# Performance work log

Hardware: AMD Instinct MI355X
Metric: run time of the kernel (lower is better)

## Reference

```python
import jax, jax.numpy as jnp
import numpy as np

B, HQ, HKV, QL, SL = 2, 32, 8, 1024, 4096
HEAD_DIM, HALF, ROPE, RANK = 128, 64, 64, 512


def setup_inputs() -> dict:
    key = jax.random.key(0)
    ks = jax.random.split(key, 6)
    return {
        "Q": jax.random.normal(ks[0], (B, HQ, QL, HEAD_DIM), jnp.float32),
        "C_kv_t2": jax.random.normal(ks[1], (B, SL, RANK), jnp.float32),
        "K_rope_t2": jax.random.normal(ks[2], (B, HKV, SL, ROPE), jnp.float32),
        "U_l": jax.random.normal(ks[3], (HALF, HALF), jnp.float32) / 8.0,
        "W_UK": jax.random.normal(ks[4], (HEAD_DIM - ROPE, RANK), jnp.float32) / 8.0,
        "W_UV": jax.random.normal(ks[5], (RANK, HEAD_DIM), jnp.float32) / 8.0,
    }


def reference(Q, C_kv_t2, K_rope_t2, U_l, W_UK, W_UV):
    # --- absorb_and_score ---
    # Rotate each half of Q by U_l (applied as x @ U_l.T)
    Qx, Qy = Q[..., :HALF], Q[..., HALF:]
    Q_rot = jnp.concatenate([Qx @ U_l.T, Qy @ U_l.T], axis=-1)  # [B,HQ,QL,HEAD_DIM]
    Q_rope = Q_rot[..., :ROPE]                                   # [B,HQ,QL,ROPE]
    Q_nope = Q_rot[..., ROPE:]                                   # [B,HQ,QL,nope_dim]
    Q_abs = Q_nope @ W_UK                                        # [B,HQ,QL,RANK]
    scores_nope = jnp.einsum('bhqr,bsr->bhqs', Q_abs, C_kv_t2)   # [B,HQ,QL,SL]
    # GQA: group q-heads per kv-head instead of materializing repeat_interleave
    g = HQ // HKV
    Qr_g = Q_rope.reshape(B, HKV, g, QL, ROPE)
    scores_rope = jnp.einsum('bkgqr,bksr->bkgqs', Qr_g, K_rope_t2)
    scores = scores_nope + scores_rope.reshape(B, HQ, QL, SL)
    # --- softmax glue + decompress_value ---
    weights = jax.nn.softmax(scores, axis=-1)                    # [B,HQ,QL,SL]
    out_latent = jnp.einsum('bhqs,bsr->bhqr', weights, C_kv_t2)  # [B,HQ,QL,RANK]
    out = out_latent @ W_UV                                      # [B,HQ,QL,HEAD_DIM]
    return out
```

## Files before the change

kernel.cpp:

```cpp
#include <hip/hip_runtime.h>
#include <stdint.h>

#define B_N   2
#define HQ_N  32
#define HKV_N 8
#define QL_N  1024
#define SL_N  4096
#define DH_N  128
#define ROPE_N 64
#define RANK_N 512

typedef _Float16 f16;
typedef _Float16 half8 __attribute__((ext_vector_type(8)));
typedef float floatx16 __attribute__((ext_vector_type(16)));
typedef int int2v __attribute__((ext_vector_type(2)));

union H8 { half8 h; uint64_t q[2]; };
union H4 { f16 h[4]; uint64_t q; };
union PKU { f16 h[2]; uint32_t u; };
union BFU { uint32_t u[4]; half8 h; };

__global__ __launch_bounds__(256) void k_convert(const float* __restrict__ C,
                                                 const float* __restrict__ Kr,
                                                 f16* __restrict__ Cf,
                                                 f16* __restrict__ Krf) {
  const size_t NC = (size_t)B_N * SL_N * RANK_N;
  size_t idx = ((size_t)blockIdx.x * 256 + threadIdx.x) * 8;
  const float* src;
  f16* dst;
  if (idx < NC) { src = C + idx;        dst = Cf + idx; }
  else          { src = Kr + (idx - NC); dst = Krf + (idx - NC); }
  float4 a = *(const float4*)(src);
  float4 b = *(const float4*)(src + 4);
  H8 o;
  o.h[0] = (f16)a.x; o.h[1] = (f16)a.y; o.h[2] = (f16)a.z; o.h[3] = (f16)a.w;
  o.h[4] = (f16)b.x; o.h[5] = (f16)b.y; o.h[6] = (f16)b.z; o.h[7] = (f16)b.w;
  *(half8*)dst = o.h;
}

__global__ __launch_bounds__(256) void k_m2(const float* __restrict__ Ul,
                                            f16* __restrict__ M2T2) {
  int idx = blockIdx.x * 256 + threadIdx.x;
  int c = idx >> 7, d = idx & 127;
  float v = 0.f;
  if (c < 64) { if (d >= 64) v = Ul[c * 64 + (d - 64)]; }
  else        { if (d < 64)  v = Ul[(c - 64) * 64 + d]; }
  M2T2[idx] = (f16)v;
}

__global__ __launch_bounds__(256) void k_qeff(const float* __restrict__ Q,
                                              const f16* __restrict__ M2T2,
                                              f16* __restrict__ Qeff2) {
  __shared__ __align__(16) f16 qs[128 * 132];
  int t = threadIdx.x;
  int wave = t >> 6, lane = t & 63, l31 = lane & 31, lhi = lane >> 5;
  size_t m0 = (size_t)blockIdx.x * 128;
#pragma unroll
  for (int i = 0; i < 16; i++) {
    int flat = i * 256 + t; int row = flat >> 5, seg = flat & 31;
    float4 v = *(const float4*)(Q + (m0 + row) * DH_N + seg * 4);
    H4 o; o.h[0] = (f16)v.x; o.h[1] = (f16)v.y; o.h[2] = (f16)v.z; o.h[3] = (f16)v.w;
    *(uint64_t*)(qs + row * 132 + seg * 4) = o.q;
  }
  __syncthreads();
  floatx16 acc[4];
#pragma unroll
  for (int ct = 0; ct < 4; ct++)
#pragma unroll
    for (int r = 0; r < 16; r++) acc[ct][r] = 0.f;
#pragma unroll
  for (int kk = 0; kk < 8; ++kk) {
    H8 af;
    const uint64_t* pa = (const uint64_t*)(qs + (wave * 32 + l31) * 132 + kk * 16 + lhi * 8);
    af.q[0] = pa[0]; af.q[1] = pa[1];
#pragma unroll
    for (int ct = 0; ct < 4; ct++) {
      H8 bf; bf.h = *(const half8*)(M2T2 + (size_t)(ct * 32 + l31) * 128 + kk * 16 + lhi * 8);
      acc[ct] = __builtin_amdgcn_mfma_f32_32x32x16_f16(af.h, bf.h, acc[ct], 0, 0, 0);
    }
  }
#pragma unroll
  for (int ct = 0; ct < 4; ct++)
#pragma unroll
    for (int r = 0; r < 16; r++) {
      int row = (r & 3) + 8 * (r >> 2) + 4 * lhi;
      Qeff2[(m0 + wave * 32 + row) * 128 + ct * 32 + l31] = (f16)acc[ct][r];
    }
}

__global__ __launch_bounds__(256) void k_kn(const f16* __restrict__ Cf,
                                            const float* __restrict__ WUK,
                                            f16* __restrict__ Kn) {
  int t = threadIdx.x;
  int wave = t >> 6, lane = t & 63, l31 = lane & 31, lhi = lane >> 5;
  int b = blockIdx.x >> 5, st = blockIdx.x & 31;
  int s0 = st * 128;
  const f16* Cb = Cf + ((size_t)b * SL_N + s0 + wave * 32) * RANK_N;
  floatx16 acc[2];
#pragma unroll
  for (int ct = 0; ct < 2; ct++)
#pragma unroll
    for (int r = 0; r < 16; r++) acc[ct][r] = 0.f;
#pragma unroll 4
  for (int kk = 0; kk < 32; ++kk) {
    H8 af; af.h = *(const half8*)(Cb + (size_t)l31 * RANK_N + kk * 16 + lhi * 8);
#pragma unroll
    for (int ct = 0; ct < 2; ct++) {
      const float* wrow = WUK + (size_t)(ct * 32 + l31) * RANK_N + kk * 16 + lhi * 8;
      float4 w0 = *(const float4*)(wrow);
      float4 w1 = *(const float4*)(wrow + 4);
      H8 bf;
      bf.h[0] = (f16)w0.x; bf.h[1] = (f16)w0.y; bf.h[2] = (f16)w0.z; bf.h[3] = (f16)w0.w;
      bf.h[4] = (f16)w1.x; bf.h[5] = (f16)w1.y; bf.h[6] = (f16)w1.z; bf.h[7] = (f16)w1.w;
      acc[ct] = __builtin_amdgcn_mfma_f32_32x32x16_f16(af.h, bf.h, acc[ct], 0, 0, 0);
    }
  }
#pragma unroll
  for (int ct = 0; ct < 2; ct++)
#pragma unroll
    for (int r = 0; r < 16; r++) {
      int row = (r & 3) + 8 * (r >> 2) + 4 * lhi;
      Kn[((size_t)b * SL_N + s0 + wave * 32 + row) * 64 + ct * 32 + l31] = (f16)acc[ct][r];
    }
}

__global__ __launch_bounds__(256) void k_cw(const f16* __restrict__ Cf,
                                            const float* __restrict__ WUV,
                                            f16* __restrict__ CWT) {
  __shared__ float ot[32 * 132];
  int t = threadIdx.x;
  int wave = t >> 6, lane = t & 63, l31 = lane & 31, lhi = lane >> 5;
  int b = blockIdx.x >> 7, st = blockIdx.x & 127;
  int s0 = st * 32;
  const f16* Cb = Cf + ((size_t)b * SL_N + s0) * RANK_N;
  floatx16 acc;
#pragma unroll
  for (int r = 0; r < 16; r++) acc[r] = 0.f;
#pragma unroll 4
  for (int kk = 0; kk < 32; ++kk) {
    H8 af; af.h = *(const half8*)(Cb + (size_t)l31 * RANK_N + kk * 16 + lhi * 8);
    H8 bf;
#pragma unroll
    for (int j = 0; j < 8; j++)
      bf.h[j] = (f16)WUV[(size_t)(kk * 16 + lhi * 8 + j) * DH_N + wave * 32 + l31];
    acc = __builtin_amdgcn_mfma_f32_32x32x16_f16(af.h, bf.h, acc, 0, 0, 0);
  }
#pragma unroll
  for (int r = 0; r < 16; r++)
    ot[((r & 3) + 8 * (r >> 2) + 4 * lhi) * 132 + wave * 32 + l31] = acc[r];
  __syncthreads();
  int c = t >> 1, sh = t & 1;
  H8 o0, o1;
#pragma unroll
  for (int j = 0; j < 8; j++) o0.h[j] = (f16)ot[(sh * 16 + j) * 132 + c];
#pragma unroll
  for (int j = 0; j < 8; j++) o1.h[j] = (f16)ot[(sh * 16 + 8 + j) * 132 + c];
  f16* dst = CWT + ((size_t)b * DH_N + c) * SL_N + s0 + sh * 16;
  *(half8*)dst = o0.h;
  *(half8*)(dst + 8) = o1.h;
}

#define KROW 132
#define CROW 36

__global__ __launch_bounds__(256, 2) void k_flash(
    const f16* __restrict__ Qeff2, const f16* __restrict__ Kn,
    const f16* __restrict__ Krf, const f16* __restrict__ CWT,
    float* __restrict__ out) {
  __shared__ __align__(16) char smem[34048];
  f16* kbuf  = (f16*)smem;
  f16* cbuf0 = (f16*)(smem + 8448);
  f16* cbuf1 = (f16*)(smem + 17664);
  float* ot  = (float*)smem;

  int t = threadIdx.x;
  int wave = t >> 6, lane = t & 63, l31 = lane & 31, lhi = lane >> 5;
  int qt = blockIdx.x & 7; int h = (blockIdx.x >> 3) & 31; int b = blockIdx.x >> 8;
  int kv = h >> 2;
  int qloc = wave * 32 + l31;

  const f16* Knb = Kn + (size_t)b * SL_N * 64;
  const f16* Kb  = Krf + (size_t)(b * HKV_N + kv) * SL_N * ROPE_N;
  const f16* Wb  = CWT + (size_t)b * DH_N * SL_N;

  half8 qf[8];
  {
    const f16* qrow = Qeff2 + ((size_t)(b * HQ_N + h) * QL_N + qt * 128 + qloc) * 128 + lhi * 8;
#pragma unroll
    for (int kk = 0; kk < 8; kk++) qf[kk] = *(const half8*)(qrow + kk * 16);
  }

  floatx16 oacc[4];
#pragma unroll
  for (int ct = 0; ct < 4; ct++)
#pragma unroll
    for (int r = 0; r < 16; r++) oacc[ct][r] = 0.f;
  float m_run = -1e30f, l_run = 0.f;

  int kr = t >> 3, kc = t & 7;
  int cA = t >> 2, cch = t & 3;

  {
    H8 kn0, rp, c0, c1;
    kn0.h = *(const half8*)(Knb + (size_t)kr * 64 + kc * 8);
    rp.h  = *(const half8*)(Kb + (size_t)kr * ROPE_N + kc * 8);
    c0.h  = *(const half8*)(Wb + (size_t)cA * SL_N + cch * 8);
    c1.h  = *(const half8*)(Wb + (size_t)(64 + cA) * SL_N + cch * 8);
    uint64_t* d0 = (uint64_t*)(kbuf + kr * KROW + kc * 8);
    d0[0] = kn0.q[0]; d0[1] = kn0.q[1];
    uint64_t* d1 = (uint64_t*)(kbuf + kr * KROW + 64 + kc * 8);
    d1[0] = rp.q[0]; d1[1] = rp.q[1];
    uint64_t* e0 = (uint64_t*)(cbuf0 + cA * CROW + cch * 8);
    e0[0] = c0.q[0]; e0[1] = c0.q[1];
    uint64_t* e1 = (uint64_t*)(cbuf0 + (64 + cA) * CROW + cch * 8);
    e1[0] = c1.q[0]; e1[1] = c1.q[1];
  }
  __syncthreads();

  for (int it = 0; it < 128; ++it) {
    f16* cc = (it & 1) ? cbuf1 : cbuf0;
    f16* cn = (it & 1) ? cbuf0 : cbuf1;
    bool pre = (it + 1) < 128;
    int s0n = (it + 1) * 32;
    H8 kn1, rp, c0, c1;
    if (pre) {
      kn1.h = *(const half8*)(Knb + (size_t)(s0n + kr) * 64 + kc * 8);
      rp.h  = *(const half8*)(Kb + (size_t)(s0n + kr) * ROPE_N + kc * 8);
      c0.h  = *(const half8*)(Wb + (size_t)cA * SL_N + s0n + cch * 8);
      c1.h  = *(const half8*)(Wb + (size_t)(64 + cA) * SL_N + s0n + cch * 8);
    }

    floatx16 sa;
#pragma unroll
    for (int r = 0; r < 16; r++) sa[r] = 0.f;
    const f16* ka = kbuf + l31 * KROW + lhi * 8;
#pragma unroll
    for (int kk = 0; kk < 8; kk++) {
      H8 a0;
      const uint64_t* p0 = (const uint64_t*)(ka + kk * 16);
      a0.q[0] = p0[0]; a0.q[1] = p0[1];
      sa = __builtin_amdgcn_mfma_f32_32x32x16_f16(a0.h, qf[kk], sa, 0, 0, 0);
    }
    __syncthreads();

    float mt = -1e30f;
#pragma unroll
    for (int r = 0; r < 16; r++) mt = fmaxf(mt, sa[r]);
    mt = fmaxf(mt, __shfl_xor(mt, 32, 64));
    if (__any(mt > m_run)) {
      float m_new = fmaxf(m_run, mt);
      float alpha = __expf(m_run - m_new);
      l_run *= alpha;
#pragma unroll
      for (int ct = 0; ct < 4; ct++)
#pragma unroll
        for (int r = 0; r < 16; r++) oacc[ct][r] *= alpha;
      m_run = m_new;
    }
    float psum = 0.f;
#pragma unroll
    for (int r = 0; r < 16; r++) { sa[r] = __expf(sa[r] - m_run); psum += sa[r]; }
    psum += __shfl_xor(psum, 32, 64);
    l_run += psum;

    uint32_t pk[8];
#pragma unroll
    for (int g = 0; g < 8; ++g) {
      PKU pu; pu.h[0] = (f16)sa[2 * g]; pu.h[1] = (f16)sa[2 * g + 1];
      pk[g] = pu.u;
    }
    {
      int2v r0 = __builtin_amdgcn_permlane32_swap((int)pk[0], (int)pk[2], false, false);
      pk[0] = (uint32_t)r0.x; pk[2] = (uint32_t)r0.y;
      int2v r1 = __builtin_amdgcn_permlane32_swap((int)pk[1], (int)pk[3], false, false);
      pk[1] = (uint32_t)r1.x; pk[3] = (uint32_t)r1.y;
      int2v r2 = __builtin_amdgcn_permlane32_swap((int)pk[4], (int)pk[6], false, false);
      pk[4] = (uint32_t)r2.x; pk[6] = (uint32_t)r2.y;
      int2v r3 = __builtin_amdgcn_permlane32_swap((int)pk[5], (int)pk[7], false, false);
      pk[5] = (uint32_t)r3.x; pk[7] = (uint32_t)r3.y;
    }
    BFU b0f, b1f;
    b0f.u[0] = pk[0]; b0f.u[1] = pk[1]; b0f.u[2] = pk[2]; b0f.u[3] = pk[3];
    b1f.u[0] = pk[4]; b1f.u[1] = pk[5]; b1f.u[2] = pk[6]; b1f.u[3] = pk[7];

#pragma unroll
    for (int ks = 0; ks < 2; ++ks) {
      half8 bfh = ks ? b1f.h : b0f.h;
#pragma unroll
      for (int ct = 0; ct < 4; ct++) {
        H8 af;
        const uint64_t* pa = (const uint64_t*)(cc + (ct * 32 + l31) * CROW + ks * 16 + lhi * 8);
        af.q[0] = pa[0]; af.q[1] = pa[1];
        oacc[ct] = __builtin_amdgcn_mfma_f32_32x32x16_f16(af.h, bfh, oacc[ct], 0, 0, 0);
      }
    }

    if (pre) {
      uint64_t* d0 = (uint64_t*)(kbuf + kr * KROW + kc * 8);
      d0[0] = kn1.q[0]; d0[1] = kn1.q[1];
      uint64_t* d1 = (uint64_t*)(kbuf + kr * KROW + 64 + kc * 8);
      d1[0] = rp.q[0]; d1[1] = rp.q[1];
      uint64_t* e0 = (uint64_t*)(cn + cA * CROW + cch * 8);
      e0[0] = c0.q[0]; e0[1] = c0.q[1];
      uint64_t* e1 = (uint64_t*)(cn + (64 + cA) * CROW + cch * 8);
      e1[0] = c1.q[0]; e1[1] = c1.q[1];
    }
    __syncthreads();
  }

  float inv = 1.0f / l_run;
  float* outp = out + ((size_t)(b * HQ_N + h) * QL_N + qt * 128) * DH_N;
#pragma unroll
  for (int p = 0; p < 2; ++p) {
    __syncthreads();
    if ((qloc >> 6) == p) {
      int lr = qloc & 63;
#pragma unroll
      for (int ct = 0; ct < 4; ct++)
#pragma unroll
        for (int r = 0; r < 16; r++) {
          int c = ct * 32 + (r & 3) + 8 * (r >> 2) + 4 * lhi;
          ot[lr * 133 + c] = oacc[ct][r] * inv;
        }
    }
    __syncthreads();
#pragma unroll
    for (int i = 0; i < 8; i++) {
      int flat = i * 256 + t; int q = flat >> 5, ch = flat & 31;
      float4 v;
      v.x = ot[q * 133 + ch * 4 + 0];
      v.y = ot[q * 133 + ch * 4 + 1];
      v.z = ot[q * 133 + ch * 4 + 2];
      v.w = ot[q * 133 + ch * 4 + 3];
      *(float4*)(outp + (size_t)(p * 64 + q) * DH_N + ch * 4) = v;
    }
  }
}

extern "C" void kernel_launch(void* const* d_in, const int* in_sizes, int n_in,
                              void* d_out, int out_size, void* d_ws, size_t ws_size,
                              hipStream_t stream) {
  (void)in_sizes; (void)n_in; (void)out_size; (void)ws_size;
  const float* Q   = (const float*)d_in[0];
  const float* C   = (const float*)d_in[1];
  const float* Kr  = (const float*)d_in[2];
  const float* Ul  = (const float*)d_in[3];
  const float* WUK = (const float*)d_in[4];
  const float* WUV = (const float*)d_in[5];
  float* out = (float*)d_out;
  char* ws = (char*)d_ws;
  f16* Qeff2 = (f16*)ws;
  f16* Cf    = (f16*)(ws + 16777216);
  f16* Krf   = (f16*)(ws + 25165824);
  f16* CWT   = (f16*)(ws + 33554432);
  f16* Kn    = (f16*)(ws + 35651584);
  f16* M2T2  = (f16*)(ws + 36700160);

  hipLaunchKernelGGL(k_convert, dim3(4096), dim3(256), 0, stream, C, Kr, Cf, Krf);
  hipLaunchKernelGGL(k_m2,      dim3(64),   dim3(256), 0, stream, Ul, M2T2);
  hipLaunchKernelGGL(k_qeff,    dim3(512),  dim3(256), 0, stream, Q, M2T2, Qeff2);
  hipLaunchKernelGGL(k_kn,      dim3(64),   dim3(256), 0, stream, Cf, WUK, Kn);
  hipLaunchKernelGGL(k_cw,      dim3(256),  dim3(256), 0, stream, Cf, WUV, CWT);
  hipLaunchKernelGGL(k_flash,   dim3(512),  dim3(256), 0, stream, Qeff2, Kn, Krf, CWT, out);
}
```

Baseline: 338.0 us.

## Load K fragments straight to registers, pre-convert weights, fold log2e into Q

The flash kernel now loads the K (nope and rope) MFMA operand fragments directly from global memory into double-buffered registers. This drops the shared-memory K buffer and one barrier per iteration, and the loop is unrolled by two to ping-pong the register sets. Q is prescaled by log2(e) so the softmax uses exp2f instead of __expf, and Q stores are staged through LDS for coalesced writes. W_UK and W_UV are converted to fp16 (W_UV transposed) once in a merged weights kernel, so k_kn and k_cw do vector fp16 loads instead of strided fp32 gathers. The cost is higher register pressure and uncoalesced per-lane K loads from global/L2.

```diff
diff --git a/kernel.cpp b/kernel.cpp
--- a/kernel.cpp
+++ b/kernel.cpp
@@ -38,14 +38,27 @@
   *(half8*)dst = o.h;
 }
 
-__global__ __launch_bounds__(256) void k_m2(const float* __restrict__ Ul,
-                                            f16* __restrict__ M2T2) {
+__global__ __launch_bounds__(256) void k_weights(const float* __restrict__ Ul,
+                                                 const float* __restrict__ WUK,
+                                                 const float* __restrict__ WUV,
+                                                 f16* __restrict__ M2T2,
+                                                 f16* __restrict__ WUKh,
+                                                 f16* __restrict__ WUVT) {
   int idx = blockIdx.x * 256 + threadIdx.x;
-  int c = idx >> 7, d = idx & 127;
-  float v = 0.f;
-  if (c < 64) { if (d >= 64) v = Ul[c * 64 + (d - 64)]; }
-  else        { if (d < 64)  v = Ul[(c - 64) * 64 + d]; }
-  M2T2[idx] = (f16)v;
+  if (idx < 16384) {
+    int c = idx >> 7, d = idx & 127;
+    float v = 0.f;
+    if (c < 64) { if (d >= 64) v = Ul[c * 64 + (d - 64)]; }
+    else        { if (d < 64)  v = Ul[(c - 64) * 64 + d]; }
+    M2T2[idx] = (f16)v;
+  } else if (idx < 49152) {
+    int i = idx - 16384;
+    WUKh[i] = (f16)WUK[i];
+  } else {
+    int i = idx - 49152;
+    int c = i >> 9, r = i & 511;
+    WUVT[i] = (f16)WUV[r * 128 + c];
+  }
 }
 
 __global__ __launch_bounds__(256) void k_qeff(const float* __restrict__ Q,
@@ -79,17 +92,28 @@
       acc[ct] = __builtin_amdgcn_mfma_f32_32x32x16_f16(af.h, bf.h, acc[ct], 0, 0, 0);
     }
   }
+  __syncthreads();
+  const float LOG2E = 1.44269504f;
 #pragma unroll
   for (int ct = 0; ct < 4; ct++)
 #pragma unroll
     for (int r = 0; r < 16; r++) {
       int row = (r & 3) + 8 * (r >> 2) + 4 * lhi;
-      Qeff2[(m0 + wave * 32 + row) * 128 + ct * 32 + l31] = (f16)acc[ct][r];
-    }
+      qs[(wave * 32 + row) * 132 + ct * 32 + l31] = (f16)(acc[ct][r] * LOG2E);
+    }
+  __syncthreads();
+#pragma unroll
+  for (int i = 0; i < 8; i++) {
+    int flat = i * 256 + t; int row = flat >> 4, ch = flat & 15;
+    const uint64_t* src = (const uint64_t*)(qs + row * 132 + ch * 8);
+    uint64_t v0 = src[0], v1 = src[1];
+    uint64_t* gd = (uint64_t*)(Qeff2 + (m0 + row) * 128 + ch * 8);
+    gd[0] = v0; gd[1] = v1;
+  }
 }
 
 __global__ __launch_bounds__(256) void k_kn(const f16* __restrict__ Cf,
-                                            const float* __restrict__ WUK,
+                                            const f16* __restrict__ WUKh,
                                             f16* __restrict__ Kn) {
   int t = threadIdx.x;
   int wave = t >> 6, lane = t & 63, l31 = lane & 31, lhi = lane >> 5;
@@ -106,12 +130,7 @@
     H8 af; af.h = *(const half8*)(Cb + (size_t)l31 * RANK_N + kk * 16 + lhi * 8);
 #pragma unroll
     for (int ct = 0; ct < 2; ct++) {
-      const float* wrow = WUK + (size_t)(ct * 32 + l31) * RANK_N + kk * 16 + lhi * 8;
-      float4 w0 = *(const float4*)(wrow);
-      float4 w1 = *(const float4*)(wrow + 4);
-      H8 bf;
-      bf.h[0] = (f16)w0.x; bf.h[1] = (f16)w0.y; bf.h[2] = (f16)w0.z; bf.h[3] = (f16)w0.w;
-      bf.h[4] = (f16)w1.x; bf.h[5] = (f16)w1.y; bf.h[6] = (f16)w1.z; bf.h[7] = (f16)w1.w;
+      H8 bf; bf.h = *(const half8*)(WUKh + (size_t)(ct * 32 + l31) * RANK_N + kk * 16 + lhi * 8);
       acc[ct] = __builtin_amdgcn_mfma_f32_32x32x16_f16(af.h, bf.h, acc[ct], 0, 0, 0);
     }
   }
@@ -125,7 +144,7 @@
 }
 
 __global__ __launch_bounds__(256) void k_cw(const f16* __restrict__ Cf,
-                                            const float* __restrict__ WUV,
+                                            const f16* __restrict__ WUVT,
                                             f16* __restrict__ CWT) {
   __shared__ float ot[32 * 132];
   int t = threadIdx.x;
@@ -139,10 +158,7 @@
 #pragma unroll 4
   for (int kk = 0; kk < 32; ++kk) {
     H8 af; af.h = *(const half8*)(Cb + (size_t)l31 * RANK_N + kk * 16 + lhi * 8);
-    H8 bf;
-#pragma unroll
-    for (int j = 0; j < 8; j++)
-      bf.h[j] = (f16)WUV[(size_t)(kk * 16 + lhi * 8 + j) * DH_N + wave * 32 + l31];
+    H8 bf; bf.h = *(const half8*)(WUVT + (size_t)(wave * 32 + l31) * RANK_N + kk * 16 + lhi * 8);
     acc = __builtin_amdgcn_mfma_f32_32x32x16_f16(af.h, bf.h, acc, 0, 0, 0);
   }
 #pragma unroll
@@ -160,7 +176,6 @@
   *(half8*)(dst + 8) = o1.h;
 }
 
-#define KROW 132
 #define CROW 36
 
 __global__ __launch_bounds__(256, 2) void k_flash(
@@ -168,9 +183,8 @@
     const f16* __restrict__ Krf, const f16* __restrict__ CWT,
     float* __restrict__ out) {
   __shared__ __align__(16) char smem[34048];
-  f16* kbuf  = (f16*)smem;
-  f16* cbuf0 = (f16*)(smem + 8448);
-  f16* cbuf1 = (f16*)(smem + 17664);
+  f16* cbuf0 = (f16*)smem;
+  f16* cbuf1 = (f16*)(smem + 9216);
   float* ot  = (float*)smem;
 
   int t = threadIdx.x;
@@ -197,19 +211,22 @@
     for (int r = 0; r < 16; r++) oacc[ct][r] = 0.f;
   float m_run = -1e30f, l_run = 0.f;
 
-  int kr = t >> 3, kc = t & 7;
   int cA = t >> 2, cch = t & 3;
-
+  const f16* pKn = Knb + (size_t)l31 * 64 + lhi * 8;
+  const f16* pKr = Kb  + (size_t)l31 * 64 + lhi * 8;
+  const f16* pW0 = Wb + (size_t)cA * SL_N + cch * 8;
+  const f16* pW1 = Wb + (size_t)(64 + cA) * SL_N + cch * 8;
+
+  H8 kA[8], kB[8];
+#pragma unroll
+  for (int kk = 0; kk < 4; kk++) {
+    kA[kk].h     = *(const half8*)(pKn + kk * 16);
+    kA[4 + kk].h = *(const half8*)(pKr + kk * 16);
+  }
   {
-    H8 kn0, rp, c0, c1;
-    kn0.h = *(const half8*)(Knb + (size_t)kr * 64 + kc * 8);
-    rp.h  = *(const half8*)(Kb + (size_t)kr * ROPE_N + kc * 8);
-    c0.h  = *(const half8*)(Wb + (size_t)cA * SL_N + cch * 8);
-    c1.h  = *(const half8*)(Wb + (size_t)(64 + cA) * SL_N + cch * 8);
-    uint64_t* d0 = (uint64_t*)(kbuf + kr * KROW + kc * 8);
-    d0[0] = kn0.q[0]; d0[1] = kn0.q[1];
-    uint64_t* d1 = (uint64_t*)(kbuf + kr * KROW + 64 + kc * 8);
-    d1[0] = rp.q[0]; d1[1] = rp.q[1];
+    H8 c0, c1;
+    c0.h = *(const half8*)(pW0);
+    c1.h = *(const half8*)(pW1);
     uint64_t* e0 = (uint64_t*)(cbuf0 + cA * CROW + cch * 8);
     e0[0] = c0.q[0]; e0[1] = c0.q[1];
     uint64_t* e1 = (uint64_t*)(cbuf0 + (64 + cA) * CROW + cch * 8);
@@ -217,31 +234,27 @@
   }
   __syncthreads();
 
-  for (int it = 0; it < 128; ++it) {
-    f16* cc = (it & 1) ? cbuf1 : cbuf0;
-    f16* cn = (it & 1) ? cbuf0 : cbuf1;
-    bool pre = (it + 1) < 128;
+  auto step = [&](H8 (&kcur)[8], H8 (&knxt)[8], f16* cc, f16* cn, int it) {
+    bool pre = it < 127;
     int s0n = (it + 1) * 32;
-    H8 kn1, rp, c0, c1;
+    H8 c0, c1;
     if (pre) {
-      kn1.h = *(const half8*)(Knb + (size_t)(s0n + kr) * 64 + kc * 8);
-      rp.h  = *(const half8*)(Kb + (size_t)(s0n + kr) * ROPE_N + kc * 8);
-      c0.h  = *(const half8*)(Wb + (size_t)cA * SL_N + s0n + cch * 8);
-      c1.h  = *(const half8*)(Wb + (size_t)(64 + cA) * SL_N + s0n + cch * 8);
+      size_t koff = (size_t)s0n * 64;
+#pragma unroll
+      for (int kk = 0; kk < 4; kk++) {
+        knxt[kk].h     = *(const half8*)(pKn + koff + kk * 16);
+        knxt[4 + kk].h = *(const half8*)(pKr + koff + kk * 16);
+      }
+      c0.h = *(const half8*)(pW0 + s0n);
+      c1.h = *(const half8*)(pW1 + s0n);
     }
 
     floatx16 sa;
 #pragma unroll
     for (int r = 0; r < 16; r++) sa[r] = 0.f;
-    const f16* ka = kbuf + l31 * KROW + lhi * 8;
-#pragma unroll
-    for (int kk = 0; kk < 8; kk++) {
-      H8 a0;
-      const uint64_t* p0 = (const uint64_t*)(ka + kk * 16);
-      a0.q[0] = p0[0]; a0.q[1] = p0[1];
-      sa = __builtin_amdgcn_mfma_f32_32x32x16_f16(a0.h, qf[kk], sa, 0, 0, 0);
-    }
-    __syncthreads();
+#pragma unroll
+    for (int kk = 0; kk < 8; kk++)
+      sa = __builtin_amdgcn_mfma_f32_32x32x16_f16(kcur[kk].h, qf[kk], sa, 0, 0, 0);
 
     float mt = -1e30f;
 #pragma unroll
@@ -249,7 +262,7 @@
     mt = fmaxf(mt, __shfl_xor(mt, 32, 64));
     if (__any(mt > m_run)) {
       float m_new = fmaxf(m_run, mt);
-      float alpha = __expf(m_run - m_new);
+      float alpha = exp2f(m_run - m_new);
       l_run *= alpha;
 #pragma unroll
       for (int ct = 0; ct < 4; ct++)
@@ -259,7 +272,7 @@
     }
     float psum = 0.f;
 #pragma unroll
-    for (int r = 0; r < 16; r++) { sa[r] = __expf(sa[r] - m_run); psum += sa[r]; }
+    for (int r = 0; r < 16; r++) { sa[r] = exp2f(sa[r] - m_run); psum += sa[r]; }
     psum += __shfl_xor(psum, 32, 64);
     l_run += psum;
 
@@ -296,16 +309,17 @@
     }
 
     if (pre) {
-      uint64_t* d0 = (uint64_t*)(kbuf + kr * KROW + kc * 8);
-      d0[0] = kn1.q[0]; d0[1] = kn1.q[1];
-      uint64_t* d1 = (uint64_t*)(kbuf + kr * KROW + 64 + kc * 8);
-      d1[0] = rp.q[0]; d1[1] = rp.q[1];
       uint64_t* e0 = (uint64_t*)(cn + cA * CROW + cch * 8);
       e0[0] = c0.q[0]; e0[1] = c0.q[1];
       uint64_t* e1 = (uint64_t*)(cn + (64 + cA) * CROW + cch * 8);
       e1[0] = c1.q[0]; e1[1] = c1.q[1];
     }
     __syncthreads();
+  };
+
+  for (int it2 = 0; it2 < 64; ++it2) {
+    step(kA, kB, cbuf0, cbuf1, 2 * it2);
+    step(kB, kA, cbuf1, cbuf0, 2 * it2 + 1);
   }
 
   float inv = 1.0f / l_run;
@@ -355,11 +369,13 @@
   f16* CWT   = (f16*)(ws + 33554432);
   f16* Kn    = (f16*)(ws + 35651584);
   f16* M2T2  = (f16*)(ws + 36700160);
+  f16* WUKh  = (f16*)(ws + 36732928);
+  f16* WUVT  = (f16*)(ws + 36798464);
 
   hipLaunchKernelGGL(k_convert, dim3(4096), dim3(256), 0, stream, C, Kr, Cf, Krf);
-  hipLaunchKernelGGL(k_m2,      dim3(64),   dim3(256), 0, stream, Ul, M2T2);
+  hipLaunchKernelGGL(k_weights, dim3(448),  dim3(256), 0, stream, Ul, WUK, WUV, M2T2, WUKh, WUVT);
   hipLaunchKernelGGL(k_qeff,    dim3(512),  dim3(256), 0, stream, Q, M2T2, Qeff2);
-  hipLaunchKernelGGL(k_kn,      dim3(64),   dim3(256), 0, stream, Cf, WUK, Kn);
-  hipLaunchKernelGGL(k_cw,      dim3(256),  dim3(256), 0, stream, Cf, WUV, CWT);
+  hipLaunchKernelGGL(k_kn,      dim3(64),   dim3(256), 0, stream, Cf, WUKh, Kn);
+  hipLaunchKernelGGL(k_cw,      dim3(256),  dim3(256), 0, stream, Cf, WUVT, CWT);
   hipLaunchKernelGGL(k_flash,   dim3(512),  dim3(256), 0, stream, Qeff2, Kn, Krf, CWT, out);
 }
```

Result: slower. 402.7 us (+19.1%).
